# Performance work log

Hardware: AMD Instinct MI355X
Metric: run time of the kernel (lower is better)

The kernel has to match this reference:

```python
import jax, jax.numpy as jnp
import numpy as np

L = 28          # num_hidden_layers (kv_cache leading dim = 2*L = 56)
H = 1024        # hidden_size
NH = 8          # num_attention_heads
KVH = 4         # num_key_value_heads
HD = 128        # head_dim
I = 3072        # mlp intermediate size
VC = 4096       # codec vocab size
NCG = 16        # num_code_groups
B = 4
S = 512         # cached seq len
THETA = 1000000.0
EPS = 1e-6


def rmsnorm(x, w):
    v = jnp.mean(jnp.square(x.astype(jnp.float32)), axis=-1, keepdims=True)
    return (x * jax.lax.rsqrt(v + EPS)).astype(x.dtype) * w


def rotate_half(x):
    h = x.shape[-1] // 2
    return jnp.concatenate([-x[..., h:], x[..., :h]], axis=-1)


def setup_inputs() -> dict:
    key = jax.random.key(0)
    ks = jax.random.split(key, 16)
    def f(k, shp, s=0.02):
        return jax.random.normal(k, shp, jnp.float32) * s
    return {
        "cb0_id": jax.random.randint(ks[0], (B, 1), 0, VC),
        "cb1_15_ids": jax.random.randint(ks[1], (B, NCG - 1), 0, VC),
        "trailing_text_embed": f(ks[2], (B, 1, H), 1.0),
        "kv_cache": f(ks[3], (2 * L, B, KVH, S, HD), 1.0),
        "position": jnp.full((B,), S, dtype=jnp.int32),
        "cb0_emb": f(ks[4], (VC, H), 1.0),
        "cp_emb": f(ks[5], (NCG - 1, VC, H), 1.0),
        "Wq": f(ks[6], (L, H, NH * HD)),
        "Wk": f(ks[7], (L, H, KVH * HD)),
        "Wv": f(ks[8], (L, H, KVH * HD)),
        "Wo": f(ks[9], (L, NH * HD, H)),
        "q_norm_w": jnp.ones((L, HD), jnp.float32),
        "k_norm_w": jnp.ones((L, HD), jnp.float32),
        "ln1_w": jnp.ones((L, H), jnp.float32),
        "ln2_w": jnp.ones((L, H), jnp.float32),
        "Wgate": f(ks[10], (L, H, I)),
        "Wup": f(ks[11], (L, H, I)),
        "Wdown": f(ks[12], (L, I, H)),
        "norm_w": jnp.ones((H,), jnp.float32),
        "head_w": f(ks[13], (H, VC)),
    }


def reference(cb0_id, cb1_15_ids, trailing_text_embed, kv_cache, position,
              cb0_emb, cp_emb, Wq, Wk, Wv, Wo, q_norm_w, k_norm_w,
              ln1_w, ln2_w, Wgate, Wup, Wdown, norm_w, head_w):
    n_rep = NH // KVH
    scale = 1.0 / np.sqrt(HD).astype(np.float32)

    # --- codebook embedding sum ---
    e = cb0_emb[cb0_id[:, 0]]                                   # [B,H]
    cp = cp_emb[jnp.arange(NCG - 1)[None, :], cb1_15_ids]       # [B,15,H]
    h = (e + cp.sum(axis=1))[:, None, :] + trailing_text_embed  # [B,1,H]

    # --- rotary at current position; broadcast shape [B,1,1,HD] ---
    inv_freq = 1.0 / (THETA ** (jnp.arange(0, HD, 2, dtype=jnp.float32) / HD))
    freqs = position.astype(jnp.float32)[:, None] * inv_freq[None, :]  # [B,HD/2]
    emb = jnp.concatenate([freqs, freqs], axis=-1)              # [B,HD]
    cos = jnp.cos(emb)[:, None, None, :]
    sin = jnp.sin(emb)[:, None, None, :]

    kv = kv_cache.reshape(L, 2, B, KVH, S, HD)

    def layer(hs, xs):
        wq, wk, wv, wo, qn, kn, l1, l2, wg, wu, wd, kc, vc = xs
        x = rmsnorm(hs, l1)
        q = (x @ wq).reshape(B, 1, NH, HD)
        k = (x @ wk).reshape(B, 1, KVH, HD)
        v = (x @ wv).reshape(B, 1, KVH, HD)
        q = jnp.transpose(rmsnorm(q, qn), (0, 2, 1, 3))   # [B,NH,1,HD]
        k = jnp.transpose(rmsnorm(k, kn), (0, 2, 1, 3))   # [B,KVH,1,HD]
        v = jnp.transpose(v, (0, 2, 1, 3))
        q = q * cos + rotate_half(q) * sin
        k = k * cos + rotate_half(k) * sin
        fk = jnp.concatenate([kc, k], axis=2)             # [B,KVH,S+1,HD]
        fv = jnp.concatenate([vc, v], axis=2)
        # GQA: head h attends kv head h // n_rep == reshape grouping (q_len = 1)
        qg = q.reshape(B, KVH, n_rep, HD)
        scores = jnp.einsum('bgrd,bgsd->bgrs', qg, fk) * scale
        w = jax.nn.softmax(scores.astype(jnp.float32), axis=-1).astype(q.dtype)
        o = jnp.einsum('bgrs,bgsd->bgrd', w, fv).reshape(B, 1, NH * HD)
        hs = hs + o @ wo
        x = rmsnorm(hs, l2)
        hs = hs + (jax.nn.silu(x @ wg) * (x @ wu)) @ wd
        return hs, (k, v)

    xs = (Wq, Wk, Wv, Wo, q_norm_w, k_norm_w, ln1_w, ln2_w,
          Wgate, Wup, Wdown, kv[:, 0], kv[:, 1])
    h, (new_k, new_v) = jax.lax.scan(layer, h, xs)

    h = rmsnorm(h, norm_w)
    past_hidden = h                                       # [B,1,H]
    logits = (h @ head_w)[:, 0, :]                        # [B,VC]

    full_k = jnp.concatenate([kv[:, 0], new_k], axis=3)   # [L,B,KVH,S+1,HD]
    full_v = jnp.concatenate([kv[:, 1], new_v], axis=3)
    new_kv_cache = jnp.stack([full_k, full_v], axis=1).reshape(2 * L, B, KVH, S + 1, HD)
    return logits, new_kv_cache, past_hidden
```

## Files before the change

### kernel.cpp

```cpp
#include <hip/hip_runtime.h>
#include <math.h>

#define L_  28
#define H_  1024
#define NH_ 8
#define KVH_ 4
#define HD_ 128
#define I_  3072
#define VC_ 4096
#define B_  4
#define S_  512
#define EPS_ 1e-6f

#define WS_HA    0
#define WS_HB    4096
#define WS_XFU   8192
#define WS_SSQ1  12288
#define WS_SSQ2  12416
#define WS_SSQF  12544
#define WS_QKVP  12672
#define WS_ATTO  274816
#define WS_ATML  340352
#define WS_OPP   341376
#define WS_GUP   472448
#define WS_DWP   1258880
#define WS_HDP   1455488

typedef float v4f __attribute__((ext_vector_type(4)));

__device__ __forceinline__ float4 ntld4(const float* p) {
    v4f r = __builtin_nontemporal_load(reinterpret_cast<const v4f*>(p));
    return make_float4(r.x, r.y, r.z, r.w);
}
__device__ __forceinline__ void ntst4(float* p, float4 v) {
    v4f r = {v.x, v.y, v.z, v.w};
    __builtin_nontemporal_store(r, reinterpret_cast<v4f*>(p));
}

__device__ __forceinline__ float wave_reduce_sum(float v) {
    #pragma unroll
    for (int off = 32; off; off >>= 1) v += __shfl_down(v, off);
    return v;
}
__device__ __forceinline__ float wave_reduce_max(float v) {
    #pragma unroll
    for (int off = 32; off; off >>= 1) v = fmaxf(v, __shfl_down(v, off));
    return v;
}

template<int RPW, int NTOT, typename F>
__device__ __forceinline__ void gemv_core(
    const float* __restrict__ W, int ldw, int wcol0, int k0,
    float* __restrict__ xsl, float4* __restrict__ accbuf,
    float* __restrict__ pp, int colblk, int ks, F&& prologue)
{
    const int t = threadIdx.x;
    const int wv = t >> 6, lane = t & 63;
    const float* Wp = W + (size_t)(k0 + wv * RPW) * ldw + wcol0 + lane * 4;
    float4 wreg[RPW];
    #pragma unroll
    for (int i = 0; i < RPW; i++) wreg[i] = ntld4(Wp + (size_t)i * ldw);
    prologue();
    const float4* xs4 = (const float4*)xsl;
    float4 a0 = {0,0,0,0}, a1 = {0,0,0,0}, a2 = {0,0,0,0}, a3 = {0,0,0,0};
    #pragma unroll
    for (int i = 0; i < RPW; i++) {
        float4 w4 = wreg[i];
        float4 xb = xs4[wv * RPW + i];
        a0.x += w4.x * xb.x; a0.y += w4.y * xb.x; a0.z += w4.z * xb.x; a0.w += w4.w * xb.x;
        a1.x += w4.x * xb.y; a1.y += w4.y * xb.y; a1.z += w4.z * xb.y; a1.w += w4.w * xb.y;
        a2.x += w4.x * xb.z; a2.y += w4.y * xb.z; a2.z += w4.z * xb.z; a2.w += w4.w * xb.z;
        a3.x += w4.x * xb.w; a3.y += w4.y * xb.w; a3.z += w4.z * xb.w; a3.w += w4.w * xb.w;
    }
    accbuf[(wv * 64 + lane) * 4 + 0] = a0;
    accbuf[(wv * 64 + lane) * 4 + 1] = a1;
    accbuf[(wv * 64 + lane) * 4 + 2] = a2;
    accbuf[(wv * 64 + lane) * 4 + 3] = a3;
    __syncthreads();
    const int l2 = t >> 2, b2 = t & 3;
    float4 s0 = accbuf[(0 * 64 + l2) * 4 + b2];
    float4 s1 = accbuf[(1 * 64 + l2) * 4 + b2];
    float4 s2 = accbuf[(2 * 64 + l2) * 4 + b2];
    float4 s3 = accbuf[(3 * 64 + l2) * 4 + b2];
    float4 s;
    s.x = s0.x + s1.x + s2.x + s3.x;
    s.y = s0.y + s1.y + s2.y + s3.y;
    s.z = s0.z + s1.z + s2.z + s3.z;
    s.w = s0.w + s1.w + s2.w + s3.w;
    *(float4*)(pp + ((size_t)ks * 4 + b2) * NTOT + colblk * 256 + l2 * 4) = s;
}

template<bool FIRST>
__global__ __launch_bounds__(256) void k_qkv(
    const float* __restrict__ hPrev, const float* __restrict__ dwp,
    const int* __restrict__ cb0, const int* __restrict__ cb1,
    const float* __restrict__ trail, const float* __restrict__ cb0e,
    const float* __restrict__ cpe,
    const float* __restrict__ ln1,
    const float* __restrict__ Wq, const float* __restrict__ Wk,
    const float* __restrict__ Wv,
    float* __restrict__ hA, float* __restrict__ ssqp1, float* __restrict__ qkvp)
{
    __shared__ float xsl[128];
    __shared__ float4 accbuf[1024];
    __shared__ float sred[128];
    const int t = threadIdx.x;
    const int ks = blockIdx.y, k0 = ks * 32, cb = blockIdx.x;
    const float* W; int ldw, wcol0;
    if (cb < 4)      { W = Wq; ldw = 1024; wcol0 = cb * 256; }
    else if (cb < 6) { W = Wk; ldw = 512;  wcol0 = (cb - 4) * 256; }
    else             { W = Wv; ldw = 512;  wcol0 = (cb - 6) * 256; }
    gemv_core<8, 2048>(W, ldw, wcol0, k0, xsl, accbuf, qkvp, cb, ks, [&]() {
        if (t < 128) {
            const int row = t >> 2, b = t & 3;
            const int gr = k0 + row;
            float hn;
            if (FIRST) {
                hn = cb0e[(size_t)cb0[b] * 1024 + gr] + trail[b * 1024 + gr];
                #pragma unroll
                for (int j = 0; j < 15; j++)
                    hn += cpe[((size_t)j * 4096 + cb1[b * 15 + j]) * 1024 + gr];
            } else {
                hn = hPrev[b * 1024 + gr];
                #pragma unroll 16
                for (int c = 0; c < 48; c++) hn += dwp[(size_t)(c * 4 + b) * 1024 + gr];
            }
            sred[t] = hn * hn;
            xsl[row * 4 + b] = hn * ln1[gr];
            if (cb == 0) hA[b * 1024 + gr] = hn;
        }
        __syncthreads();
        if (cb == 0 && t < 4) {
            float s = 0.f;
            #pragma unroll
            for (int r = 0; r < 32; r++) s += sred[r * 4 + t];
            ssqp1[ks * 4 + t] = s;
        }
    });
}

__global__ __launch_bounds__(256) void k_attn(
    const float* __restrict__ qkvp, const float* __restrict__ ssqp1,
    const float* __restrict__ qnw, const float* __restrict__ knw,
    const float* __restrict__ kin, const float* __restrict__ vin,
    float* __restrict__ kout, float* __restrict__ vout,
    const int* __restrict__ pos,
    float* __restrict__ opart, float* __restrict__ mlpart)
{
    __shared__ float Kl[33][129];
    __shared__ float Vl[33][129];
    __shared__ float ql[2][128];
    __shared__ float sc[2][36];
    __shared__ float red[8];
    __shared__ float rms1sh;

    const int t = threadIdx.x;
    const int bg = blockIdx.x, b = bg >> 2, g = bg & 3;
    const int c = blockIdx.y;
    const int lane = t & 63;
    const int r = t >> 7, d = t & 127;
    const float scale = 0.088388347648318447f;

    if (c == 15 && t == 0) {
        float s = 0.f;
        #pragma unroll
        for (int i = 0; i < 32; i++) s += ssqp1[i * 4 + b];
        rms1sh = rsqrtf(s * (1.f / 1024.f) + EPS_);
    }

    const float posf = (float)pos[b];
    const int j = d & 63;
    const float invf = exp2f(-(float)j * 0.31143075889569021f);
    const float ang = posf * invf;
    const float cs = cosf(ang), sn = sinf(ang);
    const int pd = (d < 64) ? d + 64 : d - 64;

    float qraw = 0.f;
    {
        const int n = (2 * g + r) * 128 + d;
        #pragma unroll
        for (int cc = 0; cc < 32; cc++) qraw += qkvp[((size_t)cc * 4 + b) * 2048 + n];
    }
    ql[r][d] = qraw;
    float ssq = wave_reduce_sum(qraw * qraw);
    if (lane == 0) red[t >> 6] = ssq;
    __syncthreads();
    const float rms_q = rsqrtf((red[r * 2] + red[r * 2 + 1]) * (1.f / 128.f) + EPS_);
    float qv = qraw * rms_q * qnw[d];
    float qp = ql[r][pd] * rms_q * qnw[pd];
    float qro = qv * cs + ((d < 64) ? -qp : qp) * sn;

    float kvraw = 0.f;
    if (c == 15) {
        const int base = (t < 128) ? (1024 + g * 128 + d) : (1536 + g * 128 + d);
        #pragma unroll
        for (int cc = 0; cc < 32; cc++) kvraw += qkvp[((size_t)cc * 4 + b) * 2048 + base];
    }
    float kss = wave_reduce_sum((t < 128) ? kvraw * kvraw : 0.f);
    __syncthreads();
    ql[r][d] = qro;
    if (lane == 0 && t < 128) red[t >> 6] = kss;
    if (c == 15) { if (t < 128) Kl[32][d] = kvraw; else Vl[32][d] = kvraw; }
    __syncthreads();
    float newkv = 0.f;
    if (c == 15) {
        if (t < 128) {
            const float rms_k = rsqrtf((red[0] + red[1]) * (1.f / 128.f) + EPS_);
            float kv_ = Kl[32][d] * rms_k * knw[d];
            float kp  = Kl[32][pd] * rms_k * knw[pd];
            newkv = kv_ * cs + ((d < 64) ? -kp : kp) * sn;
        } else {
            newkv = Vl[32][d] * rms1sh;
        }
    }
    __syncthreads();
    const size_t out_bg = (size_t)bg * (513 * 128);
    if (c == 15) {
        if (t < 128) { Kl[32][d] = newkv; kout[out_bg + 512 * 128 + d] = newkv; }
        else         { Vl[32][d] = newkv; vout[out_bg + 512 * 128 + d] = newkv; }
    }

    const size_t in_bg = (size_t)bg * (512 * 128);
    const int s0 = c * 32;
    #pragma unroll
    for (int i = 0; i < 4; i++) {
        int f4 = i * 256 + t;
        int row = f4 >> 5, d0 = (f4 & 31) * 4;
        float4 k4 = ntld4(kin + in_bg + (size_t)(s0 + row) * 128 + d0);
        float4 v4 = ntld4(vin + in_bg + (size_t)(s0 + row) * 128 + d0);
        Kl[row][d0] = k4.x; Kl[row][d0 + 1] = k4.y; Kl[row][d0 + 2] = k4.z; Kl[row][d0 + 3] = k4.w;
        Vl[row][d0] = v4.x; Vl[row][d0 + 1] = v4.y; Vl[row][d0 + 2] = v4.z; Vl[row][d0 + 3] = v4.w;
        ntst4(kout + out_bg + (size_t)(s0 + row) * 128 + d0, k4);
        ntst4(vout + out_bg + (size_t)(s0 + row) * 128 + d0, v4);
    }
    __syncthreads();

    const int nk = (c == 15) ? 33 : 32;
    const int si = d;
    float sv = -1e30f;
    if (si < nk) {
        float a = 0.f;
        #pragma unroll 8
        for (int dd = 0; dd < 128; dd++) a += ql[r][dd] * Kl[si][dd];
        sv = a * scale;
    }
    float mv = wave_reduce_max(sv);
    if (lane == 0) red[t >> 6] = mv;
    __syncthreads();
    const float m = fmaxf(red[r * 2], red[r * 2 + 1]);
    float p = (si < nk) ? expf(sv - m) : 0.f;
    if (si < nk) sc[r][si] = p;
    float lsum = wave_reduce_sum(p);
    __syncthreads();
    if (lane == 0) red[t >> 6] = lsum;
    __syncthreads();
    const float lr = red[r * 2] + red[r * 2 + 1];
    if (d == 0) {
        mlpart[(size_t)((bg * 2 + r) * 16 + c) * 2 + 0] = m;
        mlpart[(size_t)((bg * 2 + r) * 16 + c) * 2 + 1] = lr;
    }
    float o = 0.f;
    for (int s2 = 0; s2 < nk; s2++) o += sc[r][s2] * Vl[s2][d];
    opart[(size_t)((bg * 2 + r) * 16 + c) * 128 + d] = o;
}

__global__ __launch_bounds__(256) void k_oproj(
    const float* __restrict__ atto, const float* __restrict__ atml,
    const float* __restrict__ Wo_l, float* __restrict__ opp)
{
    __shared__ float xsl[128];
    __shared__ float4 accbuf[1024];
    const int t = threadIdx.x;
    const int ks = blockIdx.y, k0 = ks * 32, cb = blockIdx.x;
    gemv_core<8, 1024>(Wo_l, 1024, cb * 256, k0, xsl, accbuf, opp, cb, ks, [&]() {
        if (t < 128) {
            const int kk = t & 31, b = t >> 5;
            const int nrow = k0 + kk;
            const int head = nrow >> 7, dh = nrow & 127;
            const int g = head >> 1, rr = head & 1;
            const size_t base = (size_t)((b * 4 + g) * 2 + rr) * 16;
            float mc[16], lc[16], M = -1e30f;
            #pragma unroll
            for (int cc = 0; cc < 16; cc++) {
                mc[cc] = atml[(base + cc) * 2];
                lc[cc] = atml[(base + cc) * 2 + 1];
                M = fmaxf(M, mc[cc]);
            }
            float Ls = 0.f, o = 0.f;
            #pragma unroll
            for (int cc = 0; cc < 16; cc++) {
                float wch = expf(mc[cc] - M);
                Ls += lc[cc] * wch;
                o += atto[(base + cc) * 128 + dh] * wch;
            }
            xsl[kk * 4 + b] = o / Ls;
        }
        __syncthreads();
    });
}

__global__ __launch_bounds__(256) void k_gateup(
    const float* __restrict__ hA, const float* __restrict__ opp,
    const float* __restrict__ ln2,
    const float* __restrict__ Wg_l, const float* __restrict__ Wu_l,
    float* __restrict__ hB, float* __restrict__ ssqp2, float* __restrict__ gup)
{
    __shared__ float xsl[128];
    __shared__ float4 accbuf[1024];
    __shared__ float sred[128];
    const int t = threadIdx.x;
    const int ks = blockIdx.y, k0 = ks * 32, bx = blockIdx.x;
    const int wv = t >> 6, lane = t & 63;
    const int u0 = bx * 3;

    float4 wA[8], wB[8];
    {
        const float* Wp = ((u0 < 12) ? (Wg_l + u0 * 256) : (Wu_l + (u0 - 12) * 256))
                          + (size_t)(k0 + wv * 8) * 3072 + lane * 4;
        #pragma unroll
        for (int i = 0; i < 8; i++) wA[i] = ntld4(Wp + (size_t)i * 3072);
    }

    if (t < 128) {
        const int row = t >> 2, b = t & 3;
        const int gr = k0 + row;
        float hn = hA[b * 1024 + gr];
        #pragma unroll 16
        for (int c = 0; c < 32; c++) hn += opp[(size_t)(c * 4 + b) * 1024 + gr];
        sred[t] = hn * hn;
        xsl[row * 4 + b] = hn * ln2[gr];
        if (bx == 0) hB[b * 1024 + gr] = hn;
    }
    __syncthreads();
    if (bx == 0 && t < 4) {
        float s = 0.f;
        #pragma unroll
        for (int r = 0; r < 32; r++) s += sred[r * 4 + t];
        ssqp2[ks * 4 + t] = s;
    }

    const float4* xs4 = (const float4*)xsl;
    #pragma unroll
    for (int j = 0; j < 3; j++) {
        const int u = u0 + j;
        if (j < 2) {
            const int un = u0 + j + 1;
            const float* Wpn = ((un < 12) ? (Wg_l + un * 256) : (Wu_l + (un - 12) * 256))
                               + (size_t)(k0 + wv * 8) * 3072 + lane * 4;
            float4* wn = (j == 0) ? wB : wA;
            #pragma unroll
            for (int i = 0; i < 8; i++) wn[i] = ntld4(Wpn + (size_t)i * 3072);
        }
        const float4* wc = (j == 1) ? wB : wA;
        float4 a0 = {0,0,0,0}, a1 = {0,0,0,0}, a2 = {0,0,0,0}, a3 = {0,0,0,0};
        #pragma unroll
        for (int i = 0; i < 8; i++) {
            float4 w4 = wc[i];
            float4 xb = xs4[wv * 8 + i];
            a0.x += w4.x * xb.x; a0.y += w4.y * xb.x; a0.z += w4.z * xb.x; a0.w += w4.w * xb.x;
            a1.x += w4.x * xb.y; a1.y += w4.y * xb.y; a1.z += w4.z * xb.y; a1.w += w4.w * xb.y;
            a2.x += w4.x * xb.z; a2.y += w4.y * xb.z; a2.z += w4.z * xb.z; a2.w += w4.w * xb.z;
            a3.x += w4.x * xb.w; a3.y += w4.y * xb.w; a3.z += w4.z * xb.w; a3.w += w4.w * xb.w;
        }
        accbuf[(wv * 64 + lane) * 4 + 0] = a0;
        accbuf[(wv * 64 + lane) * 4 + 1] = a1;
        accbuf[(wv * 64 + lane) * 4 + 2] = a2;
        accbuf[(wv * 64 + lane) * 4 + 3] = a3;
        __syncthreads();
        const int l2 = t >> 2, b2 = t & 3;
        float4 s0 = accbuf[(0 * 64 + l2) * 4 + b2];
        float4 s1 = accbuf[(1 * 64 + l2) * 4 + b2];
        float4 s2 = accbuf[(2 * 64 + l2) * 4 + b2];
        float4 s3 = accbuf[(3 * 64 + l2) * 4 + b2];
        float4 s;
        s.x = s0.x + s1.x + s2.x + s3.x;
        s.y = s0.y + s1.y + s2.y + s3.y;
        s.z = s0.z + s1.z + s2.z + s3.z;
        s.w = s0.w + s1.w + s2.w + s3.w;
        const int ucol0 = (u < 12) ? u * 256 : 3072 + (u - 12) * 256;
        *(float4*)(gup + ((size_t)ks * 4 + b2) * 6144 + ucol0 + l2 * 4) = s;
        __syncthreads();
    }
}

__global__ __launch_bounds__(256) void k_down(
    const float* __restrict__ gup, const float* __restrict__ ssqp2,
    const float* __restrict__ Wd_l, float* __restrict__ dwp)
{
    __shared__ float xsl[256];
    __shared__ float4 accbuf[1024];
    __shared__ float rmsb[4];
    const int t = threadIdx.x;
    const int ks = blockIdx.y, k0 = ks * 64, cb = blockIdx.x;
    gemv_core<16, 1024>(Wd_l, 1024, cb * 256, k0, xsl, accbuf, dwp, cb, ks, [&]() {
        if (t < 4) {
            float s = 0.f;
            #pragma unroll
            for (int i = 0; i < 32; i++) s += ssqp2[i * 4 + t];
            rmsb[t] = rsqrtf(s * (1.f / 1024.f) + EPS_);
        }
        __syncthreads();
        const int b = t >> 6, kk = t & 63;
        const float rm = rmsb[b];
        float gg = 0.f, uu = 0.f;
        #pragma unroll 8
        for (int cc = 0; cc < 32; cc++) {
            gg += gup[((size_t)cc * 4 + b) * 6144 + k0 + kk];
            uu += gup[((size_t)cc * 4 + b) * 6144 + 3072 + k0 + kk];
        }
        gg *= rm; uu *= rm;
        xsl[kk * 4 + b] = gg / (1.f + expf(-gg)) * uu;
        __syncthreads();
    });
}

__global__ __launch_bounds__(256) void k_head(
    const float* __restrict__ hB, const float* __restrict__ dwp,
    const float* __restrict__ normw, const float* __restrict__ headw,
    float* __restrict__ xfu, float* __restrict__ ssqpF, float* __restrict__ hdp)
{
    __shared__ float xsl[128];
    __shared__ float4 accbuf[1024];
    __shared__ float sred[128];
    const int t = threadIdx.x;
    const int ks = blockIdx.y, k0 = ks * 32, cb = blockIdx.x;
    gemv_core<8, 4096>(headw, 4096, cb * 256, k0, xsl, accbuf, hdp, cb, ks, [&]() {
        if (t < 128) {
            const int row = t >> 2, b = t & 3;
            const int gr = k0 + row;
            float hn = hB[b * 1024 + gr];
            #pragma unroll 16
            for (int c = 0; c < 48; c++) hn += dwp[(size_t)(c * 4 + b) * 1024 + gr];
            sred[t] = hn * hn;
            const float x = hn * normw[gr];
            xsl[row * 4 + b] = x;
            if (cb == 0) xfu[b * 1024 + gr] = x;
        }
        __syncthreads();
        if (cb == 0 && t < 4) {
            float s = 0.f;
            #pragma unroll
            for (int r = 0; r < 32; r++) s += sred[r * 4 + t];
            ssqpF[ks * 4 + t] = s;
        }
    });
}

__global__ __launch_bounds__(256) void k_logits(
    const float* __restrict__ hdp, const float* __restrict__ ssqpF,
    const float* __restrict__ xfu,
    float* __restrict__ logits, float* __restrict__ past)
{
    __shared__ float rsh;
    const int t = threadIdx.x, bid = blockIdx.x;
    const int b = bid >> 2;
    if (t == 0) {
        float s = 0.f;
        #pragma unroll
        for (int i = 0; i < 32; i++) s += ssqpF[i * 4 + b];
        rsh = rsqrtf(s * (1.f / 1024.f) + EPS_);
    }
    __syncthreads();
    const float rf = rsh;
    const int t4 = bid * 256 + t;
    const int n4 = t4 & 1023;
    float4 s = {0.f, 0.f, 0.f, 0.f};
    #pragma unroll
    for (int c = 0; c < 32; c++) {
        float4 v = *(const float4*)(hdp + ((size_t)c * 4 + b) * 4096 + n4 * 4);
        s.x += v.x; s.y += v.y; s.z += v.z; s.w += v.w;
    }
    s.x *= rf; s.y *= rf; s.z *= rf; s.w *= rf;
    *(float4*)(logits + (size_t)t4 * 4) = s;
    if (t < 64) {
        const int p = bid * 64 + t;
        const int i4 = p & 255;
        float4 x = *(const float4*)(xfu + b * 1024 + i4 * 4);
        x.x *= rf; x.y *= rf; x.z *= rf; x.w *= rf;
        *(float4*)(past + (size_t)p * 4) = x;
    }
}

extern "C" void kernel_launch(void* const* d_in, const int* in_sizes, int n_in,
                              void* d_out, int out_size, void* d_ws, size_t ws_size,
                              hipStream_t stream)
{
    const int*   cb0   = (const int*)d_in[0];
    const int*   cb1   = (const int*)d_in[1];
    const float* trail = (const float*)d_in[2];
    const float* kvin  = (const float*)d_in[3];
    const int*   pos   = (const int*)d_in[4];
    const float* cb0e  = (const float*)d_in[5];
    const float* cpe   = (const float*)d_in[6];
    const float* Wq    = (const float*)d_in[7];
    const float* Wk    = (const float*)d_in[8];
    const float* Wv    = (const float*)d_in[9];
    const float* Wo    = (const float*)d_in[10];
    const float* qnw   = (const float*)d_in[11];
    const float* knw   = (const float*)d_in[12];
    const float* ln1   = (const float*)d_in[13];
    const float* ln2   = (const float*)d_in[14];
    const float* Wg    = (const float*)d_in[15];
    const float* Wu    = (const float*)d_in[16];
    const float* Wd    = (const float*)d_in[17];
    const float* normw = (const float*)d_in[18];
    const float* headw = (const float*)d_in[19];

    float* out    = (float*)d_out;
    float* logits = out;
    float* kvout  = out + 16384;
    float* past   = out + 16384 + (size_t)2 * L_ * B_ * KVH_ * (S_ + 1) * HD_;
    float* ws = (float*)d_ws;

    float* hA    = ws + WS_HA;
    float* hB    = ws + WS_HB;
    float* xfu   = ws + WS_XFU;
    float* ssqp1 = ws + WS_SSQ1;
    float* ssqp2 = ws + WS_SSQ2;
    float* ssqpF = ws + WS_SSQF;
    float* qkvp  = ws + WS_QKVP;
    float* atto  = ws + WS_ATTO;
    float* atml  = ws + WS_ATML;
    float* opp   = ws + WS_OPP;
    float* gup   = ws + WS_GUP;
    float* dwp   = ws + WS_DWP;
    float* hdp   = ws + WS_HDP;

    const size_t IN_PLANE  = (size_t)B_ * KVH_ * S_ * HD_;
    const size_t OUT_PLANE = (size_t)B_ * KVH_ * (S_ + 1) * HD_;

    for (int l = 0; l < L_; l++) {
        if (l == 0)
            k_qkv<true><<<dim3(8, 32), 256, 0, stream>>>(
                hB, dwp, cb0, cb1, trail, cb0e, cpe, ln1 + (size_t)l * H_,
                Wq + (size_t)l * H_ * 1024, Wk + (size_t)l * H_ * 512,
                Wv + (size_t)l * H_ * 512, hA, ssqp1, qkvp);
        else
            k_qkv<false><<<dim3(8, 32), 256, 0, stream>>>(
                hB, dwp, cb0, cb1, trail, cb0e, cpe, ln1 + (size_t)l * H_,
                Wq + (size_t)l * H_ * 1024, Wk + (size_t)l * H_ * 512,
                Wv + (size_t)l * H_ * 512, hA, ssqp1, qkvp);
        k_attn<<<dim3(16, 16), 256, 0, stream>>>(
            qkvp, ssqp1, qnw + (size_t)l * HD_, knw + (size_t)l * HD_,
            kvin + (size_t)(2 * l) * IN_PLANE, kvin + (size_t)(2 * l + 1) * IN_PLANE,
            kvout + (size_t)(2 * l) * OUT_PLANE, kvout + (size_t)(2 * l + 1) * OUT_PLANE,
            pos, atto, atml);
        k_oproj<<<dim3(4, 32), 256, 0, stream>>>(
            atto, atml, Wo + (size_t)l * 1024 * H_, opp);
        k_gateup<<<dim3(8, 32), 256, 0, stream>>>(
            hA, opp, ln2 + (size_t)l * H_,
            Wg + (size_t)l * H_ * I_, Wu + (size_t)l * H_ * I_, hB, ssqp2, gup);
        k_down<<<dim3(4, 48), 256, 0, stream>>>(
            gup, ssqp2, Wd + (size_t)l * I_ * H_, dwp);
    }
    k_head<<<dim3(16, 32), 256, 0, stream>>>(hB, dwp, normw, headw, xfu, ssqpF, hdp);
    k_logits<<<16, 256, 0, stream>>>(hdp, ssqpF, xfu, logits, past);
}
```

Baseline: 1.093 ms.

## Fuse attention combine and O-projection into gate/up kernel

Removes the separate o-projection kernel. Each gate/up block now merges the split-softmax attention partials into shared memory and computes the Wo GEMV for its own 32 hidden columns before the residual add and RMSnorm. This removes one kernel launch per layer and the partial-sum buffer round trip. In exchange, every block in the x dimension recomputes the combine and rereads its Wo slice, so Wo traffic rises eightfold with a narrow strided access pattern.

```diff
diff --git a/kernel.cpp b/kernel.cpp
--- a/kernel.cpp
+++ b/kernel.cpp
@@ -21,7 +21,6 @@
 #define WS_QKVP  12672
 #define WS_ATTO  274816
 #define WS_ATML  340352
-#define WS_OPP   341376
 #define WS_GUP   472448
 #define WS_DWP   1258880
 #define WS_HDP   1455488
@@ -264,47 +263,15 @@
     opart[(size_t)((bg * 2 + r) * 16 + c) * 128 + d] = o;
 }
 
-__global__ __launch_bounds__(256) void k_oproj(
+__global__ __launch_bounds__(256) void k_gateup(
+    const float* __restrict__ hA,
     const float* __restrict__ atto, const float* __restrict__ atml,
-    const float* __restrict__ Wo_l, float* __restrict__ opp)
-{
-    __shared__ float xsl[128];
-    __shared__ float4 accbuf[1024];
-    const int t = threadIdx.x;
-    const int ks = blockIdx.y, k0 = ks * 32, cb = blockIdx.x;
-    gemv_core<8, 1024>(Wo_l, 1024, cb * 256, k0, xsl, accbuf, opp, cb, ks, [&]() {
-        if (t < 128) {
-            const int kk = t & 31, b = t >> 5;
-            const int nrow = k0 + kk;
-            const int head = nrow >> 7, dh = nrow & 127;
-            const int g = head >> 1, rr = head & 1;
-            const size_t base = (size_t)((b * 4 + g) * 2 + rr) * 16;
-            float mc[16], lc[16], M = -1e30f;
-            #pragma unroll
-            for (int cc = 0; cc < 16; cc++) {
-                mc[cc] = atml[(base + cc) * 2];
-                lc[cc] = atml[(base + cc) * 2 + 1];
-                M = fmaxf(M, mc[cc]);
-            }
-            float Ls = 0.f, o = 0.f;
-            #pragma unroll
-            for (int cc = 0; cc < 16; cc++) {
-                float wch = expf(mc[cc] - M);
-                Ls += lc[cc] * wch;
-                o += atto[(base + cc) * 128 + dh] * wch;
-            }
-            xsl[kk * 4 + b] = o / Ls;
-        }
-        __syncthreads();
-    });
-}
-
-__global__ __launch_bounds__(256) void k_gateup(
-    const float* __restrict__ hA, const float* __restrict__ opp,
-    const float* __restrict__ ln2,
+    const float* __restrict__ Wo_l, const float* __restrict__ ln2,
     const float* __restrict__ Wg_l, const float* __restrict__ Wu_l,
     float* __restrict__ hB, float* __restrict__ ssqp2, float* __restrict__ gup)
 {
+    __shared__ float aosl[4][1024];
+    __shared__ float redsl[8][32][4];
     __shared__ float xsl[128];
     __shared__ float4 accbuf[1024];
     __shared__ float sred[128];
@@ -313,6 +280,72 @@
     const int wv = t >> 6, lane = t & 63;
     const int u0 = bx * 3;
 
+    {
+        const int b = t >> 6;
+        const int kb = (t & 63) * 16;
+        const int head = kb >> 7, dh0 = kb & 127;
+        const int g = head >> 1, rr = head & 1;
+        const size_t base = (size_t)((b * 4 + g) * 2 + rr) * 16;
+        float mc[16], lc[16], M = -1e30f;
+        #pragma unroll
+        for (int cc = 0; cc < 16; cc++) {
+            mc[cc] = atml[(base + cc) * 2];
+            lc[cc] = atml[(base + cc) * 2 + 1];
+            M = fmaxf(M, mc[cc]);
+        }
+        float Ls = 0.f, o[16];
+        #pragma unroll
+        for (int i = 0; i < 16; i++) o[i] = 0.f;
+        #pragma unroll
+        for (int cc = 0; cc < 16; cc++) {
+            const float wch = expf(mc[cc] - M);
+            Ls += lc[cc] * wch;
+            const float* ap = atto + (base + cc) * 128 + dh0;
+            #pragma unroll
+            for (int i = 0; i < 16; i++) o[i] += ap[i] * wch;
+        }
+        const float inv = 1.f / Ls;
+        #pragma unroll
+        for (int i = 0; i < 16; i++) aosl[b][kb + i] = o[i] * inv;
+    }
+    __syncthreads();
+
+    {
+        const int c = t & 31, kg = t >> 5;
+        const int col = k0 + c;
+        float a0 = 0.f, a1 = 0.f, a2 = 0.f, a3 = 0.f;
+        const float* Wp = Wo_l + (size_t)(kg * 128) * 1024 + col;
+        #pragma unroll 8
+        for (int k = 0; k < 128; k++) {
+            const float w = Wp[(size_t)k * 1024];
+            const int ka = kg * 128 + k;
+            a0 += aosl[0][ka] * w; a1 += aosl[1][ka] * w;
+            a2 += aosl[2][ka] * w; a3 += aosl[3][ka] * w;
+        }
+        redsl[kg][c][0] = a0; redsl[kg][c][1] = a1;
+        redsl[kg][c][2] = a2; redsl[kg][c][3] = a3;
+    }
+    __syncthreads();
+
+    if (t < 128) {
+        const int row = t >> 2, b = t & 3;
+        const int gr = k0 + row;
+        float op = 0.f;
+        #pragma unroll
+        for (int kg = 0; kg < 8; kg++) op += redsl[kg][row][b];
+        const float hn = hA[b * 1024 + gr] + op;
+        sred[t] = hn * hn;
+        xsl[row * 4 + b] = hn * ln2[gr];
+        if (bx == 0) hB[b * 1024 + gr] = hn;
+    }
+    __syncthreads();
+    if (bx == 0 && t < 4) {
+        float s = 0.f;
+        #pragma unroll
+        for (int r = 0; r < 32; r++) s += sred[r * 4 + t];
+        ssqp2[ks * 4 + t] = s;
+    }
+
     float4 wA[8], wB[8];
     {
         const float* Wp = ((u0 < 12) ? (Wg_l + u0 * 256) : (Wu_l + (u0 - 12) * 256))
@@ -320,25 +353,6 @@
         #pragma unroll
         for (int i = 0; i < 8; i++) wA[i] = ntld4(Wp + (size_t)i * 3072);
     }
-
-    if (t < 128) {
-        const int row = t >> 2, b = t & 3;
-        const int gr = k0 + row;
-        float hn = hA[b * 1024 + gr];
-        #pragma unroll 16
-        for (int c = 0; c < 32; c++) hn += opp[(size_t)(c * 4 + b) * 1024 + gr];
-        sred[t] = hn * hn;
-        xsl[row * 4 + b] = hn * ln2[gr];
-        if (bx == 0) hB[b * 1024 + gr] = hn;
-    }
-    __syncthreads();
-    if (bx == 0 && t < 4) {
-        float s = 0.f;
-        #pragma unroll
-        for (int r = 0; r < 32; r++) s += sred[r * 4 + t];
-        ssqp2[ks * 4 + t] = s;
-    }
-
     const float4* xs4 = (const float4*)xsl;
     #pragma unroll
     for (int j = 0; j < 3; j++) {
@@ -521,7 +535,6 @@
     float* qkvp  = ws + WS_QKVP;
     float* atto  = ws + WS_ATTO;
     float* atml  = ws + WS_ATML;
-    float* opp   = ws + WS_OPP;
     float* gup   = ws + WS_GUP;
     float* dwp   = ws + WS_DWP;
     float* hdp   = ws + WS_HDP;
@@ -545,10 +558,8 @@
             kvin + (size_t)(2 * l) * IN_PLANE, kvin + (size_t)(2 * l + 1) * IN_PLANE,
             kvout + (size_t)(2 * l) * OUT_PLANE, kvout + (size_t)(2 * l + 1) * OUT_PLANE,
             pos, atto, atml);
-        k_oproj<<<dim3(4, 32), 256, 0, stream>>>(
-            atto, atml, Wo + (size_t)l * 1024 * H_, opp);
         k_gateup<<<dim3(8, 32), 256, 0, stream>>>(
-            hA, opp, ln2 + (size_t)l * H_,
+            hA, atto, atml, Wo + (size_t)l * 1024 * H_, ln2 + (size_t)l * H_,
             Wg + (size_t)l * H_ * I_, Wu + (size_t)l * H_ * I_, hB, ssqp2, gup);
         k_down<<<dim3(4, 48), 256, 0, stream>>>(
             gup, ssqp2, Wd + (size_t)l * I_ * H_, dwp);
```

Result: slower. 1.294 ms (+18.5%).
